# Performance work log

Hardware: AMD Instinct MI355X
Metric: run time of the kernel (lower is better)

The kernel has to match this reference:

```python
import jax, jax.numpy as jnp
import numpy as np

N_NODES = 100000
N_EDGES = 1600000
NUM_FEATURES = 128
HIDDEN = 128


def _linear_init(key, fan_in, fan_out):
    kw, kb = jax.random.split(key)
    bound = 1.0 / np.sqrt(fan_in)
    w = jax.random.uniform(kw, (fan_in, fan_out), jnp.float32, -bound, bound)
    b = jax.random.uniform(kb, (fan_out,), jnp.float32, -bound, bound)
    return w, b


def setup_inputs() -> dict:
    key = jax.random.key(0)
    ks = jax.random.split(key, 8)
    x = jax.random.normal(ks[0], (N_NODES, NUM_FEATURES), jnp.float32)
    edge_index = jax.random.randint(ks[1], (2, N_EDGES), 0, N_NODES, jnp.int64)
    w11, b11 = _linear_init(ks[2], NUM_FEATURES, HIDDEN)
    w12, b12 = _linear_init(ks[3], HIDDEN, HIDDEN)
    w21, b21 = _linear_init(ks[4], HIDDEN, HIDDEN)
    w22, b22 = _linear_init(ks[5], HIDDEN, HIDDEN)
    w31, b31 = _linear_init(ks[6], HIDDEN, HIDDEN)
    w32, b32 = _linear_init(ks[7], HIDDEN, 1)
    return {"x": x, "edge_index": edge_index,
            "w11": w11, "b11": b11, "w12": w12, "b12": b12,
            "w21": w21, "b21": b21, "w22": w22, "b22": b22,
            "w31": w31, "b31": b31, "w32": w32, "b32": b32}


def _gin_conv(x, src, dst, w1, b1, w2, b2):
    # GINConv (eps=0): h_i = MLP(x_i + sum_{j->i} x_j)
    agg = jax.ops.segment_sum(x[src], dst, num_segments=N_NODES)
    h = x + agg
    h = jax.nn.relu(h @ w1 + b1)
    return h @ w2 + b2


def reference(x, edge_index, w11, b11, w12, b12, w21, b21, w22, b22, w31, b31, w32, b32):
    src, dst = edge_index[0], edge_index[1]
    h = _gin_conv(x, src, dst, w11, b11, w12, b12)
    h = _gin_conv(h, src, dst, w21, b21, w22, b22)
    h = _gin_conv(h, src, dst, w31, b31, w32, b32)  # [N, 1]
    return h
```

## Files before the change

### kernel.cpp

```cpp
#include <hip/hip_runtime.h>

#define NN 100000
#define NE 1600000
#define F 128
#define HALFN 50000
#define NBUCK ((NN + 255) >> 8)
#define SCAT_BLOCKS 512
#define EPB (NE / SCAT_BLOCKS)
#define TROWS 64
#define NTILE ((NN + TROWS - 1) / TROWS)
#define IDX_CAP 1536

typedef _Float16 f16x8 __attribute__((ext_vector_type(8)));
typedef float    f32x4 __attribute__((ext_vector_type(4)));
typedef unsigned short ushort8v __attribute__((ext_vector_type(8)));
typedef unsigned short ushort4v __attribute__((ext_vector_type(4)));

__device__ inline unsigned short f2h(float f) {
    _Float16 h = (_Float16)f;
    return __builtin_bit_cast(unsigned short, h);
}
__device__ inline float h2f(unsigned short u) {
    return (float)__builtin_bit_cast(_Float16, u);
}

__global__ __launch_bounds__(256) void k_bhist(const int* __restrict__ dst, int* __restrict__ bcnt) {
    __shared__ int sc[NBUCK];
    for (int i = threadIdx.x; i < NBUCK; i += 256) sc[i] = 0;
    __syncthreads();
    int stride = gridDim.x * 256;
    for (int e = blockIdx.x * 256 + threadIdx.x; e < NE; e += stride)
        atomicAdd(&sc[dst[e] >> 8], 1);
    __syncthreads();
    for (int i = threadIdx.x; i < NBUCK; i += 256) {
        int c = sc[i];
        if (c) atomicAdd(&bcnt[i], c);
    }
}

__global__ void k_bscan(const int* __restrict__ bcnt, int* __restrict__ bbase, int* __restrict__ bcur) {
    __shared__ int s[512];
    int t = threadIdx.x;
    int v = (t < NBUCK) ? bcnt[t] : 0;
    s[t] = v;
    __syncthreads();
    for (int off = 1; off < 512; off <<= 1) {
        int u = (t >= off) ? s[t - off] : 0;
        __syncthreads();
        s[t] += u;
        __syncthreads();
    }
    int excl = s[t] - v;
    if (t < NBUCK) { bbase[t] = excl; bcur[t] = excl; }
    if (t == 0) bbase[NBUCK] = NE;
}

__global__ __launch_bounds__(256) void k_scatterA(const int* __restrict__ src,
                                                  const int* __restrict__ dst,
                                                  int* __restrict__ bcur,
                                                  unsigned* __restrict__ scratch) {
    __shared__ uint2 sEdge[EPB];
    __shared__ int cnt[512];
    __shared__ int scn[512];
    __shared__ int cntB[512];
    __shared__ int gbase[512];
    __shared__ int ssum[256];

    const int tid = threadIdx.x;
    const int ebase = blockIdx.x * EPB;

#pragma unroll
    for (int i = tid; i < 512; i += 256) { cnt[i] = 0; cntB[i] = 0; }
    __syncthreads();

    for (int i = tid; i < EPB; i += 256) {
        int b = dst[ebase + i] >> 8;
        atomicAdd(&cnt[b], 1);
    }
    __syncthreads();

    int c0 = cnt[2 * tid], c1 = cnt[2 * tid + 1];
    ssum[tid] = c0 + c1;
    __syncthreads();
    for (int off = 1; off < 256; off <<= 1) {
        int v = (tid >= off) ? ssum[tid - off] : 0;
        __syncthreads();
        ssum[tid] += v;
        __syncthreads();
    }
    int texcl = (tid == 0) ? 0 : ssum[tid - 1];
    scn[2 * tid] = texcl;
    scn[2 * tid + 1] = texcl + c0;
#pragma unroll
    for (int i = tid; i < NBUCK; i += 256) {
        int c = cnt[i];
        gbase[i] = c ? atomicAdd(&bcur[i], c) : 0;
    }
    __syncthreads();

    for (int i = tid; i < EPB; i += 256) {
        int s = src[ebase + i], d = dst[ebase + i];
        int b = d >> 8;
        int rank = atomicAdd(&cntB[b], 1);
        sEdge[scn[b] + rank] = make_uint2((unsigned)s, (unsigned)d);
    }
    __syncthreads();

    for (int i = tid; i < EPB; i += 256) {
        uint2 ed = sEdge[i];
        int b = (int)(ed.y >> 8);
        unsigned w = ((ed.y & 255u) << 24) | ed.x;
        scratch[gbase[b] + (i - scn[b])] = w;
    }
}

__global__ __launch_bounds__(256) void k_fillB(const int* __restrict__ bbase,
                                               const unsigned* __restrict__ scratch,
                                               int* __restrict__ row_ptr,
                                               int* __restrict__ row_split,
                                               int* __restrict__ csr) {
    __shared__ int cnt[512];
    __shared__ int cur[512];
    __shared__ int ssum[256];
    int b = blockIdx.x;
    int base = bbase[b], end = bbase[b + 1];
    int t = threadIdx.x;
    cnt[t] = 0; cnt[t + 256] = 0;
    __syncthreads();
    for (int i = base + t; i < end; i += 256) {
        unsigned w = scratch[i];
        int n = w >> 24;
        int h = (int)((w & 0xFFFFFFu) >= HALFN);
        atomicAdd(&cnt[n * 2 + h], 1);
    }
    __syncthreads();
    int c0 = cnt[2 * t], c1 = cnt[2 * t + 1];
    ssum[t] = c0 + c1;
    __syncthreads();
    for (int off = 1; off < 256; off <<= 1) {
        int u = (t >= off) ? ssum[t - off] : 0;
        __syncthreads();
        ssum[t] += u;
        __syncthreads();
    }
    int texcl = (t == 0) ? 0 : ssum[t - 1];
    int node = (b << 8) + t;
    if (node < NN) {
        row_ptr[node]   = base + texcl;
        row_split[node] = base + texcl + c0;
    }
    if (b == NBUCK - 1 && t == 0) row_ptr[NN] = NE;
    cur[2 * t] = texcl;
    cur[2 * t + 1] = texcl + c0;
    __syncthreads();
    for (int i = base + t; i < end; i += 256) {
        unsigned w = scratch[i];
        int n = w >> 24;
        int srcv = (int)(w & 0xFFFFFFu);
        int h = (int)(srcv >= HALFN);
        int p = atomicAdd(&cur[n * 2 + h], 1);
        csr[base + p] = srcv;
    }
}

__global__ __launch_bounds__(256) void k_x2h(const float* __restrict__ x, unsigned short* __restrict__ xh) {
    int j = blockIdx.x * 256 + threadIdx.x;
    int c = blockIdx.y;
    if (j >= NN) return;
    const float4* px = (const float4*)&x[(size_t)j * F + c * 32];
    unsigned short* o = &xh[((size_t)c * NN + j) * 32];
#pragma unroll
    for (int half = 0; half < 4; ++half) {
        float4 v0 = px[half * 2], v1 = px[half * 2 + 1];
        ushort8v h;
        h[0] = f2h(v0.x); h[1] = f2h(v0.y); h[2] = f2h(v0.z); h[3] = f2h(v0.w);
        h[4] = f2h(v1.x); h[5] = f2h(v1.y); h[6] = f2h(v1.z); h[7] = f2h(v1.w);
        *(ushort8v*)(o + half * 8) = h;
    }
}

struct WPack {
    const float* w[5];
    unsigned short* t[5];
};

__global__ void k_w2h(WPack p) {
    int which = blockIdx.x >> 6;
    int idx = (blockIdx.x & 63) * 256 + threadIdx.x;
    int n = idx >> 7, k = idx & 127;
    p.t[which][idx] = f2h(p.w[which][k * 128 + n]);
}

template <bool LOC>
__device__ __forceinline__ void accum1(float a[8], int st, int e,
                                       const int* __restrict__ sIdx,
                                       const int* __restrict__ gIdx,
                                       const unsigned short* __restrict__ Gc,
                                       int lofs) {
    int p = st;
    for (; p + 4 <= e; p += 4) {
        int j0 = LOC ? sIdx[p]     : gIdx[p];
        int j1 = LOC ? sIdx[p + 1] : gIdx[p + 1];
        int j2 = LOC ? sIdx[p + 2] : gIdx[p + 2];
        int j3 = LOC ? sIdx[p + 3] : gIdx[p + 3];
        ushort8v v0 = *(const ushort8v*)&Gc[(size_t)j0 * 32 + lofs];
        ushort8v v1 = *(const ushort8v*)&Gc[(size_t)j1 * 32 + lofs];
        ushort8v v2 = *(const ushort8v*)&Gc[(size_t)j2 * 32 + lofs];
        ushort8v v3 = *(const ushort8v*)&Gc[(size_t)j3 * 32 + lofs];
#pragma unroll
        for (int k = 0; k < 8; ++k)
            a[k] += (h2f(v0[k]) + h2f(v1[k])) + (h2f(v2[k]) + h2f(v3[k]));
    }
    for (; p < e; ++p) {
        int j0 = LOC ? sIdx[p] : gIdx[p];
        ushort8v v0 = *(const ushort8v*)&Gc[(size_t)j0 * 32 + lofs];
#pragma unroll
        for (int k = 0; k < 8; ++k) a[k] += h2f(v0[k]);
    }
}

__global__ __launch_bounds__(256, 8) void k_agg(const unsigned short* __restrict__ G,
                                                const int* __restrict__ row_ptr,
                                                const int* __restrict__ row_split,
                                                const int* __restrict__ csr,
                                                unsigned short* __restrict__ PART) {
    __shared__ int sRP[TROWS + 1];
    __shared__ int sSP[TROWS];
    __shared__ int sIdx[IDX_CAP];

    const int tid  = threadIdx.x;
    const int tile = blockIdx.x >> 3;
    const int cc   = blockIdx.x & 7;
    const int c    = cc & 3;
    const int hb   = cc >> 2;
    const int row0 = tile * TROWS;
    const unsigned short* Gc = G + (size_t)c * NN * 32;

    if (tid < TROWS + 1) {
        int n = row0 + tid;
        if (n > NN) n = NN;
        sRP[tid] = row_ptr[n];
    } else if (tid >= 128 && tid < 128 + TROWS) {
        int n = row0 + (tid - 128);
        sSP[tid - 128] = (n < NN) ? row_split[n] : NE;
    }
    __syncthreads();
    const int ibase = sRP[0];
    const int icnt  = sRP[TROWS] - ibase;
    const int icap  = icnt < IDX_CAP ? icnt : IDX_CAP;
    for (int i = tid; i < icap; i += 256) sIdx[i] = csr[ibase + i];
    __syncthreads();

    const int g    = tid >> 2;
    const int lofs = (tid & 3) * 8;
    const int node = row0 + g;
    if (node >= NN) return;

    float a[8] = {};
    if ((node >= HALFN) == (hb != 0)) {
        ushort8v sh = *(const ushort8v*)&Gc[(size_t)node * 32 + lofs];
#pragma unroll
        for (int k = 0; k < 8; ++k) a[k] = h2f(sh[k]);
    }

    int st, e;
    if (hb == 0) { st = sRP[g] - ibase; e = sSP[g] - ibase; }
    else         { st = sSP[g] - ibase; e = sRP[g + 1] - ibase; }
    if (e <= icap)
        accum1<true>(a, st, e, sIdx, csr + ibase, Gc, lofs);
    else
        accum1<false>(a, st, e, sIdx, csr + ibase, Gc, lofs);

    ushort8v o;
#pragma unroll
    for (int k = 0; k < 8; ++k) o[k] = f2h(a[k]);
    *(ushort8v*)&PART[((size_t)cc * NN + node) * 32 + lofs] = o;
}

template <int L3>
__global__ __launch_bounds__(256, 6) void k_mlp(const unsigned short* __restrict__ PART,
                                                const unsigned short* __restrict__ W1,
                                                const float* __restrict__ b1,
                                                const unsigned short* __restrict__ W2,
                                                const float* __restrict__ b2,
                                                const float* __restrict__ w32,
                                                const float* __restrict__ b32,
                                                unsigned short* __restrict__ H,
                                                float* __restrict__ out) {
    __shared__ __align__(16) unsigned short sA[64 * 128];

    const int tid = threadIdx.x;
    const int row0 = blockIdx.x * 64;
    const int cg   = tid >> 6;
    const int lane = tid & 63;
    const int m16  = lane & 15;
    const int quad = lane >> 4;
    const size_t H1OFF = (size_t)4 * NN * 32;

#pragma unroll
    for (int i = 0; i < 4; ++i) {
        int unit = i * 256 + tid;
        int c    = unit >> 8;
        int idx  = unit & 255;
        int node = idx >> 2;
        int q    = idx & 3;
        ushort8v o = {};
        if (row0 + node < NN) {
            size_t base = ((size_t)c * NN + row0 + node) * 32 + q * 8;
            ushort8v v0 = *(const ushort8v*)&PART[base];
            ushort8v v1 = *(const ushort8v*)&PART[H1OFF + base];
#pragma unroll
            for (int k = 0; k < 8; ++k) o[k] = f2h(h2f(v0[k]) + h2f(v1[k]));
        }
        int u = c * 4 + q;
        *(ushort8v*)&sA[node * 128 + ((u ^ (node & 15)) << 3)] = o;
    }
    __syncthreads();

    f32x4 acc[4][2] = {};
#pragma unroll
    for (int ks = 0; ks < 4; ++ks) {
        f16x8 a[4];
#pragma unroll
        for (int rt = 0; rt < 4; ++rt) {
            int rowL = rt * 16 + m16;
            int u = ks * 4 + quad;
            a[rt] = *(const f16x8*)&sA[rowL * 128 + ((u ^ (rowL & 15)) << 3)];
        }
#pragma unroll
        for (int ct = 0; ct < 2; ++ct) {
            int widx = (cg * 32 + ct * 16 + m16) * 128 + ks * 32 + quad * 8;
            f16x8 b = *(const f16x8*)&W1[widx];
#pragma unroll
            for (int rt = 0; rt < 4; ++rt)
                acc[rt][ct] = __builtin_amdgcn_mfma_f32_16x16x32_f16(a[rt], b, acc[rt][ct], 0, 0, 0);
        }
    }

    if (L3) {
        float* psf = (float*)sA;
        __syncthreads();
#pragma unroll
        for (int rt = 0; rt < 4; ++rt) {
            float s[4] = {0.f, 0.f, 0.f, 0.f};
#pragma unroll
            for (int ct = 0; ct < 2; ++ct) {
                int col = cg * 32 + ct * 16 + m16;
                float bv = b1[col];
                float wv = w32[col];
#pragma unroll
                for (int i = 0; i < 4; ++i) {
                    float v = fmaxf(acc[rt][ct][i] + bv, 0.f);
                    s[i] += v * wv;
                }
            }
#pragma unroll
            for (int i = 0; i < 4; ++i) {
#pragma unroll
                for (int mask = 1; mask < 16; mask <<= 1)
                    s[i] += __shfl_xor(s[i], mask, 64);
            }
            if (m16 == 0) {
#pragma unroll
                for (int i = 0; i < 4; ++i) {
                    int rowL = rt * 16 + quad * 4 + i;
                    psf[rowL * 4 + cg] = s[i];
                }
            }
        }
        __syncthreads();
        if (tid < 64) {
            int row = row0 + tid;
            if (row < NN)
                out[row] = (psf[tid * 4] + psf[tid * 4 + 1]) + (psf[tid * 4 + 2] + psf[tid * 4 + 3]) + b32[0];
        }
        return;
    }

    __syncthreads();
#pragma unroll
    for (int rt = 0; rt < 4; ++rt) {
#pragma unroll
        for (int ct = 0; ct < 2; ++ct) {
            int col = cg * 32 + ct * 16 + m16;
            float bv = b1[col];
#pragma unroll
            for (int i = 0; i < 4; ++i) {
                int rL = rt * 16 + quad * 4 + i;
                float v = fmaxf(acc[rt][ct][i] + bv, 0.f);
                sA[rL * 128 + (((col >> 3) ^ (rL & 15)) << 3) + (col & 7)] = f2h(v);
            }
        }
    }
    __syncthreads();

    f32x4 acc2[4][2] = {};
#pragma unroll
    for (int ks = 0; ks < 4; ++ks) {
        f16x8 a[4];
#pragma unroll
        for (int rt = 0; rt < 4; ++rt) {
            int rowL = rt * 16 + m16;
            int u = ks * 4 + quad;
            a[rt] = *(const f16x8*)&sA[rowL * 128 + ((u ^ (rowL & 15)) << 3)];
        }
#pragma unroll
        for (int ct = 0; ct < 2; ++ct) {
            int widx = (cg * 32 + ct * 16 + m16) * 128 + ks * 32 + quad * 8;
            f16x8 b = *(const f16x8*)&W2[widx];
#pragma unroll
            for (int rt = 0; rt < 4; ++rt)
                acc2[rt][ct] = __builtin_amdgcn_mfma_f32_16x16x32_f16(a[rt], b, acc2[rt][ct], 0, 0, 0);
        }
    }

    __syncthreads();
#pragma unroll
    for (int rt = 0; rt < 4; ++rt) {
#pragma unroll
        for (int ct = 0; ct < 2; ++ct) {
            int col = cg * 32 + ct * 16 + m16;
            float bv = b2[col];
#pragma unroll
            for (int i = 0; i < 4; ++i) {
                int rL = rt * 16 + quad * 4 + i;
                float v = acc2[rt][ct][i] + bv;
                sA[rL * 128 + (((col >> 3) ^ (rL & 15)) << 3) + (col & 7)] = f2h(v);
            }
        }
    }
    __syncthreads();
    {
#pragma unroll
        for (int i = 0; i < 4; ++i) {
            int unit = i * 256 + tid;
            int c    = unit >> 8;
            int idx  = unit & 255;
            int node = idx >> 2;
            int q    = idx & 3;
            int u    = c * 4 + q;
            if (row0 + node < NN)
                *(ushort8v*)&H[((size_t)c * NN + row0 + node) * 32 + q * 8] =
                    *(const ushort8v*)&sA[node * 128 + ((u ^ (node & 15)) << 3)];
        }
    }
}

static inline size_t align256(size_t x) { return (x + 255) & ~(size_t)255; }

extern "C" void kernel_launch(void* const* d_in, const int* in_sizes, int n_in,
                              void* d_out, int out_size, void* d_ws, size_t ws_size,
                              hipStream_t stream) {
    const float* x   = (const float*)d_in[0];
    const int*   ei  = (const int*)d_in[1];
    const float* w11 = (const float*)d_in[2];
    const float* b11 = (const float*)d_in[3];
    const float* w12 = (const float*)d_in[4];
    const float* b12 = (const float*)d_in[5];
    const float* w21 = (const float*)d_in[6];
    const float* b21 = (const float*)d_in[7];
    const float* w22 = (const float*)d_in[8];
    const float* b22 = (const float*)d_in[9];
    const float* w31 = (const float*)d_in[10];
    const float* b31 = (const float*)d_in[11];
    const float* w32 = (const float*)d_in[12];
    const float* b32 = (const float*)d_in[13];
    float* out = (float*)d_out;

    const int* src = ei;
    const int* dst = ei + NE;

    char* ws = (char*)d_ws;
    size_t off = 0;
    unsigned short* Abuf = (unsigned short*)(ws + off); off += align256((size_t)NN * F * 2);
    unsigned short* Bbuf = (unsigned short*)(ws + off); off += align256((size_t)NN * F * 2);
    unsigned short* PART = (unsigned short*)(ws + off); off += align256((size_t)NN * F * 2 * 2);
    int* bcnt      = (int*)(ws + off); off += align256((size_t)NBUCK * 4);
    int* bbase     = (int*)(ws + off); off += align256((size_t)(NBUCK + 1) * 4);
    int* bcur      = (int*)(ws + off); off += align256((size_t)NBUCK * 4);
    int* row_ptr   = (int*)(ws + off); off += align256((size_t)(NN + 1) * 4);
    int* row_split = (int*)(ws + off); off += align256((size_t)NN * 4);
    int* csr       = (int*)(ws + off); off += align256((size_t)NE * 4);
    unsigned* scratch = (unsigned*)(ws + off); off += align256((size_t)NE * 4);
    unsigned short* wt[5];
    for (int i = 0; i < 5; ++i) {
        wt[i] = (unsigned short*)(ws + off); off += align256((size_t)128 * 128 * 2);
    }
    (void)ws_size;

    WPack wp;
    wp.w[0] = w11; wp.w[1] = w12; wp.w[2] = w21; wp.w[3] = w22; wp.w[4] = w31;
    for (int i = 0; i < 5; ++i) wp.t[i] = wt[i];
    k_w2h<<<320, 256, 0, stream>>>(wp);
    {
        dim3 gx((NN + 255) / 256, 4);
        k_x2h<<<gx, 256, 0, stream>>>(x, Abuf);
    }

    (void)hipMemsetAsync(bcnt, 0, (size_t)NBUCK * 4, stream);
    k_bhist<<<512, 256, 0, stream>>>(dst, bcnt);
    k_bscan<<<1, 512, 0, stream>>>(bcnt, bbase, bcur);
    k_scatterA<<<SCAT_BLOCKS, 256, 0, stream>>>(src, dst, bcur, scratch);
    k_fillB<<<NBUCK, 256, 0, stream>>>(bbase, scratch, row_ptr, row_split, csr);

    const int mlpTiles = (NN + 63) / 64;
    const int aggBlocks = NTILE * 8;

    k_agg<<<aggBlocks, 256, 0, stream>>>(Abuf, row_ptr, row_split, csr, PART);
    k_mlp<0><<<mlpTiles, 256, 0, stream>>>(PART, wt[0], b11, wt[1], b12,
                                           nullptr, nullptr, Bbuf, nullptr);
    k_agg<<<aggBlocks, 256, 0, stream>>>(Bbuf, row_ptr, row_split, csr, PART);
    k_mlp<0><<<mlpTiles, 256, 0, stream>>>(PART, wt[2], b21, wt[3], b22,
                                           nullptr, nullptr, Abuf, nullptr);
    k_agg<<<aggBlocks, 256, 0, stream>>>(Abuf, row_ptr, row_split, csr, PART);
    k_mlp<1><<<mlpTiles, 256, 0, stream>>>(PART, wt[4], b31, nullptr, nullptr,
                                           w32, b32, nullptr, out);
}
```

Measured before the change: 432.9 us.

## Split CSR into separate low/high source-half arrays for aggregation

The single CSR with a per-row split point is replaced by two CSRs, one for edges whose source is in the low half of the node range and one for the high half. Each half-block in aggregation now stages only its own contiguous index range into shared memory, so IDX_CAP drops to 1024. This removes the row_split load, saves shared memory and avoids staging indices the block never uses. The histogram and scan now track low and high counts separately, and the fp16 conversions are rewritten as vector convertvector operations.

```diff
diff --git a/kernel.cpp b/kernel.cpp
--- a/kernel.cpp
+++ b/kernel.cpp
@@ -9,12 +9,13 @@
 #define EPB (NE / SCAT_BLOCKS)
 #define TROWS 64
 #define NTILE ((NN + TROWS - 1) / TROWS)
-#define IDX_CAP 1536
+#define IDX_CAP 1024
 
 typedef _Float16 f16x8 __attribute__((ext_vector_type(8)));
+typedef _Float16 half8v __attribute__((ext_vector_type(8)));
 typedef float    f32x4 __attribute__((ext_vector_type(4)));
+typedef float    float8v __attribute__((ext_vector_type(8)));
 typedef unsigned short ushort8v __attribute__((ext_vector_type(8)));
-typedef unsigned short ushort4v __attribute__((ext_vector_type(4)));
 
 __device__ inline unsigned short f2h(float f) {
     _Float16 h = (_Float16)f;
@@ -24,25 +25,33 @@
     return (float)__builtin_bit_cast(_Float16, u);
 }
 
-__global__ __launch_bounds__(256) void k_bhist(const int* __restrict__ dst, int* __restrict__ bcnt) {
-    __shared__ int sc[NBUCK];
-    for (int i = threadIdx.x; i < NBUCK; i += 256) sc[i] = 0;
+__global__ __launch_bounds__(256) void k_bhist(const int* __restrict__ src,
+                                               const int* __restrict__ dst,
+                                               int* __restrict__ bcnt2) {
+    __shared__ int sc[NBUCK * 2];
+    for (int i = threadIdx.x; i < NBUCK * 2; i += 256) sc[i] = 0;
     __syncthreads();
     int stride = gridDim.x * 256;
-    for (int e = blockIdx.x * 256 + threadIdx.x; e < NE; e += stride)
-        atomicAdd(&sc[dst[e] >> 8], 1);
-    __syncthreads();
-    for (int i = threadIdx.x; i < NBUCK; i += 256) {
+    for (int e = blockIdx.x * 256 + threadIdx.x; e < NE; e += stride) {
+        int b = dst[e] >> 8;
+        int h = (int)(src[e] >= HALFN);
+        atomicAdd(&sc[b * 2 + h], 1);
+    }
+    __syncthreads();
+    for (int i = threadIdx.x; i < NBUCK * 2; i += 256) {
         int c = sc[i];
-        if (c) atomicAdd(&bcnt[i], c);
-    }
-}
-
-__global__ void k_bscan(const int* __restrict__ bcnt, int* __restrict__ bbase, int* __restrict__ bcur) {
+        if (c) atomicAdd(&bcnt2[i], c);
+    }
+}
+
+__global__ void k_bscan(const int* __restrict__ bcnt2,
+                        int* __restrict__ bbaseL, int* __restrict__ bbaseH,
+                        int* __restrict__ bbase, int* __restrict__ bcur) {
     __shared__ int s[512];
     int t = threadIdx.x;
-    int v = (t < NBUCK) ? bcnt[t] : 0;
-    s[t] = v;
+    int vL = (t < NBUCK) ? bcnt2[2 * t] : 0;
+    int vH = (t < NBUCK) ? bcnt2[2 * t + 1] : 0;
+    s[t] = vL;
     __syncthreads();
     for (int off = 1; off < 512; off <<= 1) {
         int u = (t >= off) ? s[t - off] : 0;
@@ -50,9 +59,29 @@
         s[t] += u;
         __syncthreads();
     }
-    int excl = s[t] - v;
-    if (t < NBUCK) { bbase[t] = excl; bcur[t] = excl; }
-    if (t == 0) bbase[NBUCK] = NE;
+    int incL = s[t];
+    __syncthreads();
+    s[t] = vH;
+    __syncthreads();
+    for (int off = 1; off < 512; off <<= 1) {
+        int u = (t >= off) ? s[t - off] : 0;
+        __syncthreads();
+        s[t] += u;
+        __syncthreads();
+    }
+    int incH = s[t];
+    int exL = incL - vL, exH = incH - vH;
+    if (t < NBUCK) {
+        bbaseL[t] = exL;
+        bbaseH[t] = exH;
+        bbase[t] = exL + exH;
+        bcur[t] = exL + exH;
+    }
+    if (t == NBUCK - 1) {
+        bbaseL[NBUCK] = incL;
+        bbaseH[NBUCK] = incH;
+        bbase[NBUCK] = incL + incH;
+    }
 }
 
 __global__ __launch_bounds__(256) void k_scatterA(const int* __restrict__ src,
@@ -115,13 +144,16 @@
 }
 
 __global__ __launch_bounds__(256) void k_fillB(const int* __restrict__ bbase,
+                                               const int* __restrict__ bbaseL,
+                                               const int* __restrict__ bbaseH,
                                                const unsigned* __restrict__ scratch,
-                                               int* __restrict__ row_ptr,
-                                               int* __restrict__ row_split,
-                                               int* __restrict__ csr) {
+                                               int* __restrict__ row_ptrL,
+                                               int* __restrict__ row_ptrH,
+                                               int* __restrict__ csrL,
+                                               int* __restrict__ csrH) {
     __shared__ int cnt[512];
-    __shared__ int cur[512];
-    __shared__ int ssum[256];
+    __shared__ int sA[256];
+    __shared__ int sB[256];
     int b = blockIdx.x;
     int base = bbase[b], end = bbase[b + 1];
     int t = threadIdx.x;
@@ -135,31 +167,35 @@
     }
     __syncthreads();
     int c0 = cnt[2 * t], c1 = cnt[2 * t + 1];
-    ssum[t] = c0 + c1;
+    sA[t] = c0; sB[t] = c1;
     __syncthreads();
     for (int off = 1; off < 256; off <<= 1) {
-        int u = (t >= off) ? ssum[t - off] : 0;
-        __syncthreads();
-        ssum[t] += u;
-        __syncthreads();
-    }
-    int texcl = (t == 0) ? 0 : ssum[t - 1];
+        int uA = (t >= off) ? sA[t - off] : 0;
+        int uB = (t >= off) ? sB[t - off] : 0;
+        __syncthreads();
+        sA[t] += uA; sB[t] += uB;
+        __syncthreads();
+    }
+    int exL = sA[t] - c0, exH = sB[t] - c1;
     int node = (b << 8) + t;
     if (node < NN) {
-        row_ptr[node]   = base + texcl;
-        row_split[node] = base + texcl + c0;
-    }
-    if (b == NBUCK - 1 && t == 0) row_ptr[NN] = NE;
-    cur[2 * t] = texcl;
-    cur[2 * t + 1] = texcl + c0;
+        row_ptrL[node] = bbaseL[b] + exL;
+        row_ptrH[node] = bbaseH[b] + exH;
+    }
+    if (b == NBUCK - 1 && t == 0) {
+        row_ptrL[NN] = bbaseL[NBUCK];
+        row_ptrH[NN] = bbaseH[NBUCK];
+    }
+    cnt[2 * t] = exL; cnt[2 * t + 1] = exH;
     __syncthreads();
     for (int i = base + t; i < end; i += 256) {
         unsigned w = scratch[i];
         int n = w >> 24;
         int srcv = (int)(w & 0xFFFFFFu);
         int h = (int)(srcv >= HALFN);
-        int p = atomicAdd(&cur[n * 2 + h], 1);
-        csr[base + p] = srcv;
+        int p = atomicAdd(&cnt[n * 2 + h], 1);
+        if (h) csrH[bbaseH[b] + p] = srcv;
+        else   csrL[bbaseL[b] + p] = srcv;
     }
 }
 
@@ -192,7 +228,7 @@
 }
 
 template <bool LOC>
-__device__ __forceinline__ void accum1(float a[8], int st, int e,
+__device__ __forceinline__ void accum1(float8v& a, int st, int e,
                                        const int* __restrict__ sIdx,
                                        const int* __restrict__ gIdx,
                                        const unsigned short* __restrict__ Gc,
@@ -203,29 +239,30 @@
         int j1 = LOC ? sIdx[p + 1] : gIdx[p + 1];
         int j2 = LOC ? sIdx[p + 2] : gIdx[p + 2];
         int j3 = LOC ? sIdx[p + 3] : gIdx[p + 3];
-        ushort8v v0 = *(const ushort8v*)&Gc[(size_t)j0 * 32 + lofs];
-        ushort8v v1 = *(const ushort8v*)&Gc[(size_t)j1 * 32 + lofs];
-        ushort8v v2 = *(const ushort8v*)&Gc[(size_t)j2 * 32 + lofs];
-        ushort8v v3 = *(const ushort8v*)&Gc[(size_t)j3 * 32 + lofs];
-#pragma unroll
-        for (int k = 0; k < 8; ++k)
-            a[k] += (h2f(v0[k]) + h2f(v1[k])) + (h2f(v2[k]) + h2f(v3[k]));
+        half8v v0 = *(const half8v*)&Gc[(size_t)j0 * 32 + lofs];
+        half8v v1 = *(const half8v*)&Gc[(size_t)j1 * 32 + lofs];
+        half8v v2 = *(const half8v*)&Gc[(size_t)j2 * 32 + lofs];
+        half8v v3 = *(const half8v*)&Gc[(size_t)j3 * 32 + lofs];
+        float8v f0 = __builtin_convertvector(v0, float8v);
+        float8v f1 = __builtin_convertvector(v1, float8v);
+        float8v f2 = __builtin_convertvector(v2, float8v);
+        float8v f3 = __builtin_convertvector(v3, float8v);
+        a += (f0 + f1) + (f2 + f3);
     }
     for (; p < e; ++p) {
         int j0 = LOC ? sIdx[p] : gIdx[p];
-        ushort8v v0 = *(const ushort8v*)&Gc[(size_t)j0 * 32 + lofs];
-#pragma unroll
-        for (int k = 0; k < 8; ++k) a[k] += h2f(v0[k]);
+        half8v v0 = *(const half8v*)&Gc[(size_t)j0 * 32 + lofs];
+        a += __builtin_convertvector(v0, float8v);
     }
 }
 
 __global__ __launch_bounds__(256, 8) void k_agg(const unsigned short* __restrict__ G,
-                                                const int* __restrict__ row_ptr,
-                                                const int* __restrict__ row_split,
-                                                const int* __restrict__ csr,
+                                                const int* __restrict__ row_ptrL,
+                                                const int* __restrict__ row_ptrH,
+                                                const int* __restrict__ csrL,
+                                                const int* __restrict__ csrH,
                                                 unsigned short* __restrict__ PART) {
     __shared__ int sRP[TROWS + 1];
-    __shared__ int sSP[TROWS];
     __shared__ int sIdx[IDX_CAP];
 
     const int tid  = threadIdx.x;
@@ -235,20 +272,19 @@
     const int hb   = cc >> 2;
     const int row0 = tile * TROWS;
     const unsigned short* Gc = G + (size_t)c * NN * 32;
+    const int* __restrict__ rp = hb ? row_ptrH : row_ptrL;
+    const int* __restrict__ cs = hb ? csrH : csrL;
 
     if (tid < TROWS + 1) {
         int n = row0 + tid;
         if (n > NN) n = NN;
-        sRP[tid] = row_ptr[n];
-    } else if (tid >= 128 && tid < 128 + TROWS) {
-        int n = row0 + (tid - 128);
-        sSP[tid - 128] = (n < NN) ? row_split[n] : NE;
+        sRP[tid] = rp[n];
     }
     __syncthreads();
     const int ibase = sRP[0];
     const int icnt  = sRP[TROWS] - ibase;
     const int icap  = icnt < IDX_CAP ? icnt : IDX_CAP;
-    for (int i = tid; i < icap; i += 256) sIdx[i] = csr[ibase + i];
+    for (int i = tid; i < icap; i += 256) sIdx[i] = cs[ibase + i];
     __syncthreads();
 
     const int g    = tid >> 2;
@@ -256,25 +292,20 @@
     const int node = row0 + g;
     if (node >= NN) return;
 
-    float a[8] = {};
+    float8v a = {};
     if ((node >= HALFN) == (hb != 0)) {
-        ushort8v sh = *(const ushort8v*)&Gc[(size_t)node * 32 + lofs];
-#pragma unroll
-        for (int k = 0; k < 8; ++k) a[k] = h2f(sh[k]);
-    }
-
-    int st, e;
-    if (hb == 0) { st = sRP[g] - ibase; e = sSP[g] - ibase; }
-    else         { st = sSP[g] - ibase; e = sRP[g + 1] - ibase; }
+        half8v sh = *(const half8v*)&Gc[(size_t)node * 32 + lofs];
+        a = __builtin_convertvector(sh, float8v);
+    }
+
+    int st = sRP[g] - ibase, e = sRP[g + 1] - ibase;
     if (e <= icap)
-        accum1<true>(a, st, e, sIdx, csr + ibase, Gc, lofs);
+        accum1<true>(a, st, e, sIdx, cs + ibase, Gc, lofs);
     else
-        accum1<false>(a, st, e, sIdx, csr + ibase, Gc, lofs);
-
-    ushort8v o;
-#pragma unroll
-    for (int k = 0; k < 8; ++k) o[k] = f2h(a[k]);
-    *(ushort8v*)&PART[((size_t)cc * NN + node) * 32 + lofs] = o;
+        accum1<false>(a, st, e, sIdx, cs + ibase, Gc, lofs);
+
+    half8v o = __builtin_convertvector(a, half8v);
+    *(half8v*)&PART[((size_t)cc * NN + node) * 32 + lofs] = o;
 }
 
 template <int L3>
@@ -304,16 +335,16 @@
         int idx  = unit & 255;
         int node = idx >> 2;
         int q    = idx & 3;
-        ushort8v o = {};
+        half8v o = {};
         if (row0 + node < NN) {
             size_t base = ((size_t)c * NN + row0 + node) * 32 + q * 8;
-            ushort8v v0 = *(const ushort8v*)&PART[base];
-            ushort8v v1 = *(const ushort8v*)&PART[H1OFF + base];
-#pragma unroll
-            for (int k = 0; k < 8; ++k) o[k] = f2h(h2f(v0[k]) + h2f(v1[k]));
+            half8v v0 = *(const half8v*)&PART[base];
+            half8v v1 = *(const half8v*)&PART[H1OFF + base];
+            float8v s = __builtin_convertvector(v0, float8v) + __builtin_convertvector(v1, float8v);
+            o = __builtin_convertvector(s, half8v);
         }
         int u = c * 4 + q;
-        *(ushort8v*)&sA[node * 128 + ((u ^ (node & 15)) << 3)] = o;
+        *(half8v*)&sA[node * 128 + ((u ^ (node & 15)) << 3)] = o;
     }
     __syncthreads();
 
@@ -475,12 +506,15 @@
     unsigned short* Abuf = (unsigned short*)(ws + off); off += align256((size_t)NN * F * 2);
     unsigned short* Bbuf = (unsigned short*)(ws + off); off += align256((size_t)NN * F * 2);
     unsigned short* PART = (unsigned short*)(ws + off); off += align256((size_t)NN * F * 2 * 2);
-    int* bcnt      = (int*)(ws + off); off += align256((size_t)NBUCK * 4);
-    int* bbase     = (int*)(ws + off); off += align256((size_t)(NBUCK + 1) * 4);
-    int* bcur      = (int*)(ws + off); off += align256((size_t)NBUCK * 4);
-    int* row_ptr   = (int*)(ws + off); off += align256((size_t)(NN + 1) * 4);
-    int* row_split = (int*)(ws + off); off += align256((size_t)NN * 4);
-    int* csr       = (int*)(ws + off); off += align256((size_t)NE * 4);
+    int* bcnt2   = (int*)(ws + off); off += align256((size_t)NBUCK * 2 * 4);
+    int* bbaseL  = (int*)(ws + off); off += align256((size_t)(NBUCK + 1) * 4);
+    int* bbaseH  = (int*)(ws + off); off += align256((size_t)(NBUCK + 1) * 4);
+    int* bbase   = (int*)(ws + off); off += align256((size_t)(NBUCK + 1) * 4);
+    int* bcur    = (int*)(ws + off); off += align256((size_t)NBUCK * 4);
+    int* row_ptrL = (int*)(ws + off); off += align256((size_t)(NN + 1) * 4);
+    int* row_ptrH = (int*)(ws + off); off += align256((size_t)(NN + 1) * 4);
+    int* csrL    = (int*)(ws + off); off += align256((size_t)NE * 4);
+    int* csrH    = (int*)(ws + off); off += align256((size_t)NE * 4);
     unsigned* scratch = (unsigned*)(ws + off); off += align256((size_t)NE * 4);
     unsigned short* wt[5];
     for (int i = 0; i < 5; ++i) {
@@ -497,22 +531,23 @@
         k_x2h<<<gx, 256, 0, stream>>>(x, Abuf);
     }
 
-    (void)hipMemsetAsync(bcnt, 0, (size_t)NBUCK * 4, stream);
-    k_bhist<<<512, 256, 0, stream>>>(dst, bcnt);
-    k_bscan<<<1, 512, 0, stream>>>(bcnt, bbase, bcur);
+    (void)hipMemsetAsync(bcnt2, 0, (size_t)NBUCK * 2 * 4, stream);
+    k_bhist<<<512, 256, 0, stream>>>(src, dst, bcnt2);
+    k_bscan<<<1, 512, 0, stream>>>(bcnt2, bbaseL, bbaseH, bbase, bcur);
     k_scatterA<<<SCAT_BLOCKS, 256, 0, stream>>>(src, dst, bcur, scratch);
-    k_fillB<<<NBUCK, 256, 0, stream>>>(bbase, scratch, row_ptr, row_split, csr);
+    k_fillB<<<NBUCK, 256, 0, stream>>>(bbase, bbaseL, bbaseH, scratch,
+                                       row_ptrL, row_ptrH, csrL, csrH);
 
     const int mlpTiles = (NN + 63) / 64;
     const int aggBlocks = NTILE * 8;
 
-    k_agg<<<aggBlocks, 256, 0, stream>>>(Abuf, row_ptr, row_split, csr, PART);
+    k_agg<<<aggBlocks, 256, 0, stream>>>(Abuf, row_ptrL, row_ptrH, csrL, csrH, PART);
     k_mlp<0><<<mlpTiles, 256, 0, stream>>>(PART, wt[0], b11, wt[1], b12,
                                            nullptr, nullptr, Bbuf, nullptr);
-    k_agg<<<aggBlocks, 256, 0, stream>>>(Bbuf, row_ptr, row_split, csr, PART);
+    k_agg<<<aggBlocks, 256, 0, stream>>>(Bbuf, row_ptrL, row_ptrH, csrL, csrH, PART);
     k_mlp<0><<<mlpTiles, 256, 0, stream>>>(PART, wt[2], b21, wt[3], b22,
                                            nullptr, nullptr, Abuf, nullptr);
-    k_agg<<<aggBlocks, 256, 0, stream>>>(Abuf, row_ptr, row_split, csr, PART);
+    k_agg<<<aggBlocks, 256, 0, stream>>>(Abuf, row_ptrL, row_ptrH, csrL, csrH, PART);
     k_mlp<1><<<mlpTiles, 256, 0, stream>>>(PART, wt[4], b31, nullptr, nullptr,
                                            w32, b32, nullptr, out);
 }
```

After: 416.2 us. 1.04x faster.
